# Performance work log

Hardware: AMD Instinct MI355X
Metric: run time of the kernel (lower is better)

## Reference

```python
import jax, jax.numpy as jnp
import numpy as np

MAX_DEPTH = 8          # inner-node depths 1..8; leaves at depth 9
LMBDA = 0.1            # args.lmbda; per-node lmbda = LMBDA * 2**(-depth)
EPS = 1e-6


def setup_inputs() -> dict:
    key = jax.random.key(0)
    ks = jax.random.split(key, 7)
    B, D, O = 16384, 2048, 1000
    n_inner = 2 ** MAX_DEPTH - 1   # 255
    n_leaf = 2 ** MAX_DEPTH       # 256
    x = jax.random.normal(ks[0], (B, D), dtype=jnp.float32)
    target = jax.random.randint(ks[1], (B,), 0, O)
    y = jax.nn.one_hot(target, O, dtype=jnp.float32)  # target_onehot
    W = jax.random.normal(ks[2], (n_inner, D), dtype=jnp.float32) / np.sqrt(D)
    b = jax.random.normal(ks[3], (n_inner,), dtype=jnp.float32) * 0.01
    beta = jax.random.normal(ks[4], (n_inner,), dtype=jnp.float32)
    leaf_params = jax.random.normal(ks[5], (n_leaf, O), dtype=jnp.float32)
    return {"x": x, "y": y, "W": W, "b": b, "beta": beta, "leaf_params": leaf_params}


def reference(x, y, W, b, beta, leaf_params):
    """Faithful vectorized version of SoftDecisionTree.cal_loss.
    Inner nodes are stored in level-order (heap) layout, left-to-right
    within each level, matching the left-first recursion of cal_prob.
    Returns (loss, output) like cal_loss.
    """
    B = x.shape[0]
    dt = x.dtype
    # All inner-node gates in one fused GEMM: sigmoid(beta * (x @ w + b))
    probs = jax.nn.sigmoid(beta * (x @ W.T + b))  # [B, n_inner]

    path = jnp.ones((B, 1), dt)  # path_prob_init
    C = jnp.asarray(0.0, dt)
    idx = 0
    for d in range(1, MAX_DEPTH + 1):  # small fixed loop over tree levels
        n = 2 ** (d - 1)
        p = probs[:, idx:idx + n]      # gate probs for this level's nodes [B, n]
        if d < MAX_DEPTH:              # get_penalty skips nodes whose children are leaves
            denom = jnp.sum(path, axis=0)                  # [n]
            denom = jnp.where(denom == 0, EPS, denom)
            alpha = jnp.sum(p * path, axis=0) / denom      # [n]
            alpha = jnp.clip(alpha, EPS, 1.0 - EPS)
            lmbda = LMBDA * 2.0 ** (-d)
            C = C - jnp.sum(lmbda * 0.5 * (jnp.log(alpha) + jnp.log1p(-alpha)))
        # children: left gets path*(1-p), right gets path*p, interleaved
        path = jnp.stack([path * (1.0 - p), path * p], axis=-1).reshape(B, 2 * n)
        idx += n
    # path: [B, n_leaf] leaf arrival probabilities (left-to-right leaf order)

    logQ = jax.nn.log_softmax(leaf_params, axis=-1)  # [n_leaf, O]
    TQ = y @ logQ.T                                  # [B, n_leaf]: y . log Q per leaf
    loss_term = jnp.mean(jnp.sum(path * TQ, axis=1))
    loss = -loss_term + C

    best = jnp.argmax(path, axis=1)   # first max, matches the '<' update order
    output = jnp.exp(logQ)[best]      # [B, O] max_Q
    return loss, output
```

## Files before the change

### kernel.cpp

```cpp
#include <hip/hip_runtime.h>


typedef __attribute__((ext_vector_type(8))) short short8;
typedef __attribute__((ext_vector_type(4))) float f32x4;

#define DIM 2048
#define NCLS 1000
#define NINNER 255
#define NPAD 256

__device__ __forceinline__ unsigned cvt2bf(float a, float b) {
  return ((__float_as_uint(a) + 0x8000u) >> 16) | ((__float_as_uint(b) + 0x8000u) & 0xFFFF0000u);
}

__device__ __forceinline__ void async_copy16(const unsigned short* gsrc, unsigned short* ldst) {
  __builtin_amdgcn_global_load_lds(
      (const __attribute__((address_space(1))) unsigned int*)(gsrc),
      (__attribute__((address_space(3))) unsigned int*)(ldst), 16, 0, 0);
}

__global__ __launch_bounds__(256) void prep_w(const float* __restrict__ W,
                                              const float* __restrict__ b,
                                              const float* __restrict__ beta,
                                              unsigned short* __restrict__ Wb,
                                              float* __restrict__ bp,
                                              float* __restrict__ betap) {
  int i = blockIdx.x * 256 + threadIdx.x;
  int n = i >> 11;
  float v = (n < NINNER) ? W[i] : 0.f;
  Wb[i] = (unsigned short)((__float_as_uint(v) + 0x8000u) >> 16);
  if (i < NPAD) {
    bp[i] = (i < NINNER) ? b[i] : 0.f;
    betap[i] = (i < NINNER) ? beta[i] : 0.f;
  }
}

__global__ __launch_bounds__(256) void leaf_softmax(const float* __restrict__ leaf,
                                                    float* __restrict__ logQT,
                                                    float* __restrict__ Q) {
  int l = blockIdx.x, t = threadIdx.x;
  const float* row = leaf + (size_t)l * NCLS;
  __shared__ float red[256];
  float mx = -3.4e38f;
  for (int j = t; j < NCLS; j += 256) mx = fmaxf(mx, row[j]);
  red[t] = mx; __syncthreads();
  for (int s = 128; s; s >>= 1) { if (t < s) red[t] = fmaxf(red[t], red[t + s]); __syncthreads(); }
  mx = red[0]; __syncthreads();
  float sm = 0.f;
  for (int j = t; j < NCLS; j += 256) sm += __expf(row[j] - mx);
  red[t] = sm; __syncthreads();
  for (int s = 128; s; s >>= 1) { if (t < s) red[t] += red[t + s]; __syncthreads(); }
  float lse = mx + __logf(red[0]);
  for (int j = t; j < NCLS; j += 256) {
    float lg = row[j] - lse;
    logQT[(size_t)j * NPAD + l] = lg;
    Q[(size_t)l * NCLS + j] = __expf(lg);
  }
}

__global__ __launch_bounds__(256) void find_targets(const float* __restrict__ y,
                                                    int* __restrict__ tgt) {
  int wv = threadIdx.x >> 6, lane = threadIdx.x & 63;
  int r = blockIdx.x * 4 + wv;
  const float4* yr = (const float4*)(y + (size_t)r * NCLS);
  int found = 0x7fffffff;
#pragma unroll
  for (int i = 0; i < 4; ++i) {
    int j4 = i * 64 + lane;
    if (j4 < 250) {
      float4 v = yr[j4];
      if (v.x > 0.5f) found = min(found, 4 * j4 + 0);
      if (v.y > 0.5f) found = min(found, 4 * j4 + 1);
      if (v.z > 0.5f) found = min(found, 4 * j4 + 2);
      if (v.w > 0.5f) found = min(found, 4 * j4 + 3);
    }
  }
  for (int off = 32; off; off >>= 1) found = min(found, __shfl_down(found, off));
  if (lane == 0) tgt[r] = found;
}

__global__ __launch_bounds__(256, 2) void gemm_xwT(const float* __restrict__ x,
                                                   const unsigned short* __restrict__ Wb,
                                                   float* __restrict__ P0,
                                                   float* __restrict__ P1) {
  __shared__ __align__(16) unsigned short As[128 * 40];
  __shared__ __align__(16) unsigned short Bs[128 * 32];

  int tid = threadIdx.x;
  int lane = tid & 63, wave = tid >> 6;
  int m_base = blockIdx.x * 128;
  int n_base = blockIdx.y * 128;
  int k_base = blockIdx.z * 1024;
  float* P = blockIdx.z ? P1 : P0;

  f32x4 acc[4][4] = {};

  int arow = tid >> 1, aseg = tid & 1;
  const float* aptr = x + (size_t)(m_base + arow) * DIM + k_base + aseg * 16;
  unsigned short* asd = &As[arow * 40 + aseg * 16];

  int ci0 = wave * 2, ci1 = wave * 2 + 1;
  const unsigned short* bg0 =
      Wb + (size_t)(n_base + ci0 * 16 + (lane >> 2)) * DIM + k_base + (lane & 3) * 8;
  const unsigned short* bg1 = bg0 + (size_t)16 * DIM;
  unsigned short* bl0 = &Bs[ci0 * 512];
  unsigned short* bl1 = &Bs[ci1 * 512];

  int frow = lane & 15, fquad = lane >> 4;
  int wrow = (wave & 1) * 64;
  int wcol = (wave >> 1) * 64;

  for (int kt = 0; kt < 1024; kt += 32) {
    const float4* ap = (const float4*)(aptr + kt);
    float4 v0 = ap[0], v1 = ap[1], v2 = ap[2], v3 = ap[3];
    uint4 p0, p1;
    p0.x = cvt2bf(v0.x, v0.y); p0.y = cvt2bf(v0.z, v0.w);
    p0.z = cvt2bf(v1.x, v1.y); p0.w = cvt2bf(v1.z, v1.w);
    p1.x = cvt2bf(v2.x, v2.y); p1.y = cvt2bf(v2.z, v2.w);
    p1.z = cvt2bf(v3.x, v3.y); p1.w = cvt2bf(v3.z, v3.w);
    __syncthreads();
    *(uint4*)asd = p0;
    *(uint4*)(asd + 8) = p1;
    async_copy16(bg0 + kt, bl0);
    async_copy16(bg1 + kt, bl1);
    __syncthreads();
    short8 a[4];
#pragma unroll
    for (int mt = 0; mt < 4; ++mt)
      a[mt] = *(const short8*)&As[(wrow + mt * 16 + frow) * 40 + fquad * 8];
#pragma unroll
    for (int nt = 0; nt < 4; ++nt) {
      short8 bb = *(const short8*)&Bs[(wcol + nt * 16 + frow) * 32 + fquad * 8];
#pragma unroll
      for (int mt = 0; mt < 4; ++mt)
        acc[mt][nt] = __builtin_amdgcn_mfma_f32_16x16x32_bf16(a[mt], bb, acc[mt][nt], 0, 0, 0);
    }
  }
#pragma unroll
  for (int mt = 0; mt < 4; ++mt) {
#pragma unroll
    for (int rg = 0; rg < 4; ++rg) {
      float* dst = P + (size_t)(m_base + wrow + mt * 16 + fquad * 4 + rg) * NPAD + n_base + wcol + frow;
#pragma unroll
      for (int nt = 0; nt < 4; ++nt) dst[nt * 16] = acc[mt][nt][rg];
    }
  }
}

__global__ __launch_bounds__(256) void tree_walk(const float* __restrict__ P0,
                                                 const float* __restrict__ P1,
                                                 const float* __restrict__ bp,
                                                 const float* __restrict__ betap,
                                                 const float* __restrict__ logQT,
                                                 const int* __restrict__ tgt,
                                                 float* __restrict__ acc,
                                                 int* __restrict__ best) {
  __shared__ float ws[4][256];
  __shared__ float s0s[127], s1s[127];
  __shared__ float sdot;
  int tid = threadIdx.x;
  int lane = tid & 63, wv = tid >> 6;
  if (tid < 127) { s0s[tid] = 0.f; s1s[tid] = 0.f; }
  if (tid == 255) sdot = 0.f;
  __syncthreads();
  float4 bb = *(const float4*)(bp + lane * 4);
  float4 be = *(const float4*)(betap + lane * 4);
  float* wsp = ws[wv];
  float wdot = 0.f;
  for (int it = 0; it < 4; ++it) {
    int r = blockIdx.x * 16 + wv * 4 + it;
    float4 u = *(const float4*)(P0 + (size_t)r * NPAD + lane * 4);
    float4 v = *(const float4*)(P1 + (size_t)r * NPAD + lane * 4);
    float4 pz;
    pz.x = 1.f / (1.f + __expf(-be.x * (u.x + v.x + bb.x)));
    pz.y = 1.f / (1.f + __expf(-be.y * (u.y + v.y + bb.y)));
    pz.z = 1.f / (1.f + __expf(-be.z * (u.z + v.z + bb.z)));
    pz.w = 1.f / (1.f + __expf(-be.w * (u.w + v.w + bb.w)));
    *(float4*)(wsp + lane * 4) = pz;
    __asm__ volatile("" ::: "memory");
    int tg = tgt[r];
    float pp = 1.f;
#pragma unroll
    for (int d = 1; d <= 6; ++d) {
      int idx = (1 << (d - 1)) - 1 + (lane >> (7 - d));
      float p = wsp[idx];
      if ((lane & ((1 << (7 - d)) - 1)) == 0) {
        atomicAdd(&s0s[idx], pp);
        atomicAdd(&s1s[idx], p * pp);
      }
      pp *= ((lane >> (6 - d)) & 1) ? p : (1.f - p);
    }
    float p7 = wsp[63 + lane];
    atomicAdd(&s0s[63 + lane], pp);
    atomicAdd(&s1s[63 + lane], p7 * pp);
    float pL = pp * (1.f - p7), pR = pp * p7;
    float p8a = wsp[127 + 2 * lane], p8b = wsp[128 + 2 * lane];
    float lf0 = pL * (1.f - p8a), lf1 = pL * p8a;
    float lf2 = pR * (1.f - p8b), lf3 = pR * p8b;
    float4 lq = *(const float4*)(logQT + (size_t)tg * NPAD + lane * 4);
    wdot += lf0 * lq.x + lf1 * lq.y + lf2 * lq.z + lf3 * lq.w;
    float bv = lf0; int bi = 4 * lane;
    if (lf1 > bv) { bv = lf1; bi = 4 * lane + 1; }
    if (lf2 > bv) { bv = lf2; bi = 4 * lane + 2; }
    if (lf3 > bv) { bv = lf3; bi = 4 * lane + 3; }
    for (int off = 32; off; off >>= 1) {
      float ov = __shfl_down(bv, off);
      int oi = __shfl_down(bi, off);
      if (ov > bv || (ov == bv && oi < bi)) { bv = ov; bi = oi; }
    }
    if (lane == 0) best[r] = bi;
  }
  for (int off = 32; off; off >>= 1) wdot += __shfl_down(wdot, off);
  if (lane == 0) atomicAdd(&sdot, wdot);
  __syncthreads();
  if (tid < 127) {
    atomicAdd(&acc[tid], s0s[tid]);
    atomicAdd(&acc[127 + tid], s1s[tid]);
  }
  if (tid == 255) atomicAdd(&acc[254], sdot);
}

__global__ __launch_bounds__(128) void finalize_loss(const float* __restrict__ acc,
                                                     float* __restrict__ out) {
  __shared__ float red[128];
  int t = threadIdx.x;
  float c = 0.f;
  if (t < 127) {
    float denom = acc[t];
    if (denom == 0.f) denom = 1e-6f;
    float alpha = acc[127 + t] / denom;
    alpha = fminf(fmaxf(alpha, 1e-6f), 1.f - 1e-6f);
    int d = 31 - __clz(t + 1) + 1;
    float lm = 0.1f * exp2f(-(float)d);
    c = -lm * 0.5f * (logf(alpha) + log1pf(-alpha));
  }
  red[t] = c;
  __syncthreads();
  for (int s = 64; s; s >>= 1) { if (t < s) red[t] += red[t + s]; __syncthreads(); }
  if (t == 0) out[0] = -(acc[254] / 16384.f) + red[0];
}

__global__ __launch_bounds__(256) void gather_rows(const float* __restrict__ Q,
                                                   const int* __restrict__ best,
                                                   float* __restrict__ out) {
  int wv = threadIdx.x >> 6, lane = threadIdx.x & 63;
  int r = blockIdx.x * 4 + wv;
  const float* src = Q + (size_t)best[r] * NCLS;
  float* dst = out + 1 + (size_t)r * NCLS;
  if (lane < 3) dst[lane] = src[lane];
  if (lane == 0) dst[999] = src[999];
#pragma unroll
  for (int i = 0; i < 4; ++i) {
    int q = i * 64 + lane;
    if (q < 249) {
      int o = 3 + 4 * q;
      float4 v = make_float4(src[o], src[o + 1], src[o + 2], src[o + 3]);
      *(float4*)(dst + o) = v;
    }
  }
}

extern "C" void kernel_launch(void* const* d_in, const int* in_sizes, int n_in,
                              void* d_out, int out_size, void* d_ws, size_t ws_size,
                              hipStream_t stream) {
  const float* x = (const float*)d_in[0];
  const float* y = (const float*)d_in[1];
  const float* W = (const float*)d_in[2];
  const float* b = (const float*)d_in[3];
  const float* beta = (const float*)d_in[4];
  const float* leaf = (const float*)d_in[5];
  float* out = (float*)d_out;
  char* ws = (char*)d_ws;

  unsigned short* Wb = (unsigned short*)(ws + 0);
  float* bp    = (float*)(ws + 1048576);
  float* betap = (float*)(ws + 1049600);
  float* acc   = (float*)(ws + 1050624);
  int* tgt     = (int*)(ws + 1051648);
  int* best    = (int*)(ws + 1117184);
  float* logQT = (float*)(ws + 1182720);
  float* Q     = (float*)(ws + 2206720);
  float* P0    = (float*)(ws + 3230720);
  float* P1    = out + 4;

  prep_w<<<2048, 256, 0, stream>>>(W, b, beta, Wb, bp, betap);
  leaf_softmax<<<256, 256, 0, stream>>>(leaf, logQT, Q);
  find_targets<<<4096, 256, 0, stream>>>(y, tgt);
  gemm_xwT<<<dim3(128, 2, 2), 256, 0, stream>>>(x, Wb, P0, P1);
  hipMemsetAsync(acc, 0, 256 * sizeof(float), stream);
  tree_walk<<<1024, 256, 0, stream>>>(P0, P1, bp, betap, logQT, tgt, acc, best);
  finalize_loss<<<1, 128, 0, stream>>>(acc, out);
  gather_rows<<<4096, 256, 0, stream>>>(Q, best, out);
}
```

Measured before the change: 362.9 us.

## Retile GEMM to 64x256 tiles with 4-way split-K and swizzled B LDS

Result: no change. 365.1 us (+0.6%).

```diff
diff --git a/kernel.cpp b/kernel.cpp
--- a/kernel.cpp
+++ b/kernel.cpp
@@ -8,6 +8,7 @@
 #define NCLS 1000
 #define NINNER 255
 #define NPAD 256
+#define PSTRIDE (16384ull * NPAD)
 
 __device__ __forceinline__ unsigned cvt2bf(float a, float b) {
   return ((__float_as_uint(a) + 0x8000u) >> 16) | ((__float_as_uint(b) + 0x8000u) & 0xFFFF0000u);
@@ -79,58 +80,59 @@
   if (lane == 0) tgt[r] = found;
 }
 
-__global__ __launch_bounds__(256, 2) void gemm_xwT(const float* __restrict__ x,
+__global__ __launch_bounds__(256, 4) void gemm_xwT(const float* __restrict__ x,
                                                    const unsigned short* __restrict__ Wb,
-                                                   float* __restrict__ P0,
-                                                   float* __restrict__ P1) {
-  __shared__ __align__(16) unsigned short As[128 * 40];
-  __shared__ __align__(16) unsigned short Bs[128 * 32];
+                                                   float* __restrict__ P) {
+  __shared__ __align__(16) unsigned short As[64 * 40];
+  __shared__ __align__(16) unsigned short Bs[256 * 32];
 
   int tid = threadIdx.x;
   int lane = tid & 63, wave = tid >> 6;
-  int m_base = blockIdx.x * 128;
-  int n_base = blockIdx.y * 128;
-  int k_base = blockIdx.z * 1024;
-  float* P = blockIdx.z ? P1 : P0;
+  int m_base = blockIdx.x * 64;
+  int k_base = blockIdx.z * 512;
+  float* Pz = P + (size_t)blockIdx.z * PSTRIDE;
 
   f32x4 acc[4][4] = {};
 
-  int arow = tid >> 1, aseg = tid & 1;
-  const float* aptr = x + (size_t)(m_base + arow) * DIM + k_base + aseg * 16;
-  unsigned short* asd = &As[arow * 40 + aseg * 16];
-
-  int ci0 = wave * 2, ci1 = wave * 2 + 1;
-  const unsigned short* bg0 =
-      Wb + (size_t)(n_base + ci0 * 16 + (lane >> 2)) * DIM + k_base + (lane & 3) * 8;
-  const unsigned short* bg1 = bg0 + (size_t)16 * DIM;
-  unsigned short* bl0 = &Bs[ci0 * 512];
-  unsigned short* bl1 = &Bs[ci1 * 512];
-
-  int frow = lane & 15, fquad = lane >> 4;
-  int wrow = (wave & 1) * 64;
-  int wcol = (wave >> 1) * 64;
-
-  for (int kt = 0; kt < 1024; kt += 32) {
-    const float4* ap = (const float4*)(aptr + kt);
-    float4 v0 = ap[0], v1 = ap[1], v2 = ap[2], v3 = ap[3];
-    uint4 p0, p1;
-    p0.x = cvt2bf(v0.x, v0.y); p0.y = cvt2bf(v0.z, v0.w);
-    p0.z = cvt2bf(v1.x, v1.y); p0.w = cvt2bf(v1.z, v1.w);
-    p1.x = cvt2bf(v2.x, v2.y); p1.y = cvt2bf(v2.z, v2.w);
-    p1.z = cvt2bf(v3.x, v3.y); p1.w = cvt2bf(v3.z, v3.w);
+  int arow = tid >> 2, aseg = tid & 3;
+  const float* aptr = x + (size_t)(m_base + arow) * DIM + k_base + aseg * 8;
+  unsigned short* asd = &As[arow * 40 + aseg * 8];
+
+  int rr = lane >> 2;
+  int sg = (lane & 3) ^ ((rr + (rr >> 2)) & 3);
+  const unsigned short* bg0 = Wb + (size_t)(wave * 64 + rr) * DIM + k_base + sg * 8;
+  const unsigned short* bg1 = bg0 + 16 * DIM;
+  const unsigned short* bg2 = bg0 + 32 * DIM;
+  const unsigned short* bg3 = bg0 + 48 * DIM;
+  unsigned short* bl0 = &Bs[(wave * 4 + 0) * 512];
+  unsigned short* bl1 = &Bs[(wave * 4 + 1) * 512];
+  unsigned short* bl2 = &Bs[(wave * 4 + 2) * 512];
+  unsigned short* bl3 = &Bs[(wave * 4 + 3) * 512];
+
+  int frow = lane & 15, q = lane >> 4;
+  int bseg = (q ^ ((frow + (frow >> 2)) & 3)) * 8;
+  int wcol = wave * 64;
+
+  for (int kt = 0; kt < 512; kt += 32) {
+    float4 v0 = *(const float4*)(aptr + kt);
+    float4 v1 = *(const float4*)(aptr + kt + 4);
+    uint4 pk;
+    pk.x = cvt2bf(v0.x, v0.y); pk.y = cvt2bf(v0.z, v0.w);
+    pk.z = cvt2bf(v1.x, v1.y); pk.w = cvt2bf(v1.z, v1.w);
     __syncthreads();
-    *(uint4*)asd = p0;
-    *(uint4*)(asd + 8) = p1;
+    *(uint4*)asd = pk;
     async_copy16(bg0 + kt, bl0);
     async_copy16(bg1 + kt, bl1);
+    async_copy16(bg2 + kt, bl2);
+    async_copy16(bg3 + kt, bl3);
     __syncthreads();
     short8 a[4];
 #pragma unroll
     for (int mt = 0; mt < 4; ++mt)
-      a[mt] = *(const short8*)&As[(wrow + mt * 16 + frow) * 40 + fquad * 8];
+      a[mt] = *(const short8*)&As[(mt * 16 + frow) * 40 + q * 8];
 #pragma unroll
     for (int nt = 0; nt < 4; ++nt) {
-      short8 bb = *(const short8*)&Bs[(wcol + nt * 16 + frow) * 32 + fquad * 8];
+      short8 bb = *(const short8*)&Bs[(wcol + nt * 16 + frow) * 32 + bseg];
 #pragma unroll
       for (int mt = 0; mt < 4; ++mt)
         acc[mt][nt] = __builtin_amdgcn_mfma_f32_16x16x32_bf16(a[mt], bb, acc[mt][nt], 0, 0, 0);
@@ -140,15 +142,14 @@
   for (int mt = 0; mt < 4; ++mt) {
 #pragma unroll
     for (int rg = 0; rg < 4; ++rg) {
-      float* dst = P + (size_t)(m_base + wrow + mt * 16 + fquad * 4 + rg) * NPAD + n_base + wcol + frow;
+      float* dst = Pz + (size_t)(m_base + mt * 16 + q * 4 + rg) * NPAD + wcol + frow;
 #pragma unroll
       for (int nt = 0; nt < 4; ++nt) dst[nt * 16] = acc[mt][nt][rg];
     }
   }
 }
 
-__global__ __launch_bounds__(256) void tree_walk(const float* __restrict__ P0,
-                                                 const float* __restrict__ P1,
+__global__ __launch_bounds__(256) void tree_walk(const float* __restrict__ P,
                                                  const float* __restrict__ bp,
                                                  const float* __restrict__ betap,
                                                  const float* __restrict__ logQT,
@@ -169,13 +170,16 @@
   float wdot = 0.f;
   for (int it = 0; it < 4; ++it) {
     int r = blockIdx.x * 16 + wv * 4 + it;
-    float4 u = *(const float4*)(P0 + (size_t)r * NPAD + lane * 4);
-    float4 v = *(const float4*)(P1 + (size_t)r * NPAD + lane * 4);
+    const float* pr = P + (size_t)r * NPAD + lane * 4;
+    float4 u0 = *(const float4*)(pr);
+    float4 u1 = *(const float4*)(pr + PSTRIDE);
+    float4 u2 = *(const float4*)(pr + 2 * PSTRIDE);
+    float4 u3 = *(const float4*)(pr + 3 * PSTRIDE);
     float4 pz;
-    pz.x = 1.f / (1.f + __expf(-be.x * (u.x + v.x + bb.x)));
-    pz.y = 1.f / (1.f + __expf(-be.y * (u.y + v.y + bb.y)));
-    pz.z = 1.f / (1.f + __expf(-be.z * (u.z + v.z + bb.z)));
-    pz.w = 1.f / (1.f + __expf(-be.w * (u.w + v.w + bb.w)));
+    pz.x = 1.f / (1.f + __expf(-be.x * (u0.x + u1.x + u2.x + u3.x + bb.x)));
+    pz.y = 1.f / (1.f + __expf(-be.y * (u0.y + u1.y + u2.y + u3.y + bb.y)));
+    pz.z = 1.f / (1.f + __expf(-be.z * (u0.z + u1.z + u2.z + u3.z + bb.z)));
+    pz.w = 1.f / (1.f + __expf(-be.w * (u0.w + u1.w + u2.w + u3.w + bb.w)));
     *(float4*)(wsp + lane * 4) = pz;
     __asm__ volatile("" ::: "memory");
     int tg = tgt[r];
@@ -280,15 +284,14 @@
   int* best    = (int*)(ws + 1117184);
   float* logQT = (float*)(ws + 1182720);
   float* Q     = (float*)(ws + 2206720);
-  float* P0    = (float*)(ws + 3230720);
-  float* P1    = out + 4;
+  float* P     = (float*)(ws + 3230720);
 
   prep_w<<<2048, 256, 0, stream>>>(W, b, beta, Wb, bp, betap);
   leaf_softmax<<<256, 256, 0, stream>>>(leaf, logQT, Q);
   find_targets<<<4096, 256, 0, stream>>>(y, tgt);
-  gemm_xwT<<<dim3(128, 2, 2), 256, 0, stream>>>(x, Wb, P0, P1);
+  gemm_xwT<<<dim3(256, 1, 4), 256, 0, stream>>>(x, Wb, P);
   hipMemsetAsync(acc, 0, 256 * sizeof(float), stream);
-  tree_walk<<<1024, 256, 0, stream>>>(P0, P1, bp, betap, logQT, tgt, acc, best);
+  tree_walk<<<1024, 256, 0, stream>>>(P, bp, betap, logQT, tgt, acc, best);
   finalize_loss<<<1, 128, 0, stream>>>(acc, out);
   gather_rows<<<4096, 256, 0, stream>>>(Q, best, out);
 }
```
